# Kernel tuning notes

Hardware: AMD Instinct MI355X
Metric: run time of the kernel (lower is better)

## Reference

```python
import jax, jax.numpy as jnp
import numpy as np

VOL = (8, 56, 56)      # D, H, W
KER = (4, 7, 7)        # window size
SHIFT = (2, 3, 3)      # kernel // 2
C = 128                # embedding_dim
P = 256                # projection_dim
NH = 8                 # heads
HD = P // NH           # head dim = 32
HID = 3 * C            # mlp_ratio * C
B = 2
L = KER[0] * KER[1] * KER[2]                      # 196 tokens per window
NW = (VOL[0] // KER[0]) * (VOL[1] // KER[1]) * (VOL[2] // KER[2])  # 128 windows
EPS = 1e-5


def _rel_index():
    kd, kh, kw = KER
    coords = np.stack(np.meshgrid(np.arange(kd), np.arange(kh), np.arange(kw), indexing='ij'), 0).reshape(3, -1)
    rel = coords[:, :, None] - coords[:, None, :]
    rel = rel + np.array([kd - 1, kh - 1, kw - 1])[:, None, None]
    idx = rel[0] * (2 * kh - 1) * (2 * kw - 1) + rel[1] * (2 * kw - 1) + rel[2]
    return idx.astype(np.int32)  # [L, L]


def _shift_mask():
    D, H, W = VOL
    kd, kh, kw = KER
    sd, sh, sw = SHIFT
    img = np.zeros((D, H, W))
    cnt = 0
    for ds in (slice(0, -kd), slice(-kd, -sd), slice(-sd, None)):
        for hs in (slice(0, -kh), slice(-kh, -sh), slice(-sh, None)):
            for ws in (slice(0, -kw), slice(-kw, -sw), slice(-sw, None)):
                img[ds, hs, ws] = cnt
                cnt += 1
    win = img.reshape(D // kd, kd, H // kh, kh, W // kw, kw).transpose(0, 2, 4, 1, 3, 5).reshape(NW, L)
    diff = win[:, None, :] - win[:, :, None]
    return np.where(diff != 0, -100.0, 0.0).astype(np.float32)  # [NW, L, L]


def _partition(x):
    b = x.shape[0]
    kd, kh, kw = KER
    D, H, W = VOL
    x = x.reshape(b, D // kd, kd, H // kh, kh, W // kw, kw, C)
    x = x.transpose(0, 1, 3, 5, 2, 4, 6, 7)
    return x.reshape(b * NW, L, C)


def _reverse(x):
    b = x.shape[0] // NW
    kd, kh, kw = KER
    D, H, W = VOL
    x = x.reshape(b, D // kd, H // kh, W // kw, kd, kh, kw, C)
    x = x.transpose(0, 1, 4, 2, 5, 3, 6, 7)
    return x.reshape(b, D, H, W, C)


def _ln(x, g, b):
    mu = jnp.mean(x, -1, keepdims=True)
    var = jnp.mean(jnp.square(x - mu), -1, keepdims=True)
    return (x - mu) * jax.lax.rsqrt(var + EPS) * g + b


def setup_inputs() -> dict:
    key = jax.random.key(0)
    ks = jax.random.split(key, 16)
    s = 0.02
    d = {
        'query': jax.random.normal(ks[0], (B,) + VOL + (C,), jnp.float32),
        'key':   jax.random.normal(ks[1], (B,) + VOL + (C,), jnp.float32),
        'value': jax.random.normal(ks[2], (B,) + VOL + (C,), jnp.float32),
        'Wq': jax.random.normal(ks[3], (C, P), jnp.float32) * s,
        'bq': jnp.zeros((P,), jnp.float32),
        'Wk': jax.random.normal(ks[4], (C, P), jnp.float32) * s,
        'bk': jnp.zeros((P,), jnp.float32),
        'Wv': jax.random.normal(ks[5], (C, P), jnp.float32) * s,
        'bv': jnp.zeros((P,), jnp.float32),
        'Wo': jax.random.normal(ks[6], (P, C), jnp.float32) * s,
        'bo': jnp.zeros((C,), jnp.float32),
        'rel_table': jax.random.normal(ks[7], ((2 * KER[0] - 1) * (2 * KER[1] - 1) * (2 * KER[2] - 1), NH), jnp.float32) * s,
        'ln1_g': jnp.ones((C,), jnp.float32), 'ln1_b': jnp.zeros((C,), jnp.float32),
        'W1': jax.random.normal(ks[8], (C, HID), jnp.float32) * s,
        'b1': jnp.zeros((HID,), jnp.float32),
        'W2': jax.random.normal(ks[9], (HID, C), jnp.float32) * s,
        'b2': jnp.zeros((C,), jnp.float32),
        'ln2_g': jnp.ones((C,), jnp.float32), 'ln2_b': jnp.zeros((C,), jnp.float32),
        'rel_idx': jnp.asarray(_rel_index()),
        'attn_mask': jnp.asarray(_shift_mask()),
    }
    return d


def reference(query, key, value, Wq, bq, Wk, bk, Wv, bv, Wo, bo, rel_table,
              ln1_g, ln1_b, W1, b1, W2, b2, ln2_g, ln2_b, rel_idx, attn_mask):
    sd, sh, sw = SHIFT
    ax = (1, 2, 3)
    q = _partition(jnp.roll(query, (-sd, -sh, -sw), ax))
    k = _partition(jnp.roll(key,   (-sd, -sh, -sw), ax))
    v = _partition(jnp.roll(value, (-sd, -sh, -sw), ax))
    residual = q
    Bn = q.shape[0]
    qh = (q @ Wq + bq).reshape(Bn, L, NH, HD).transpose(0, 2, 1, 3)
    kh = (k @ Wk + bk).reshape(Bn, L, NH, HD).transpose(0, 2, 1, 3)
    vh = (v @ Wv + bv).reshape(Bn, L, NH, HD).transpose(0, 2, 1, 3)
    logits = jnp.einsum('bhqd,bhkd->bhqk', qh, kh) * (HD ** -0.5)
    bias = rel_table[rel_idx]                       # [L, L, NH]
    logits = logits + bias.transpose(2, 0, 1)[None]
    logits = logits.reshape(Bn // NW, NW, NH, L, L) + attn_mask[None, :, None]
    probs = jax.nn.softmax(logits.reshape(Bn, NH, L, L), axis=-1)
    ctx = jnp.einsum('bhqk,bhkd->bhqd', probs, vh).transpose(0, 2, 1, 3).reshape(Bn, L, P)
    attn = ctx @ Wo + bo
    attn = _ln(attn, ln1_g, ln1_b) + residual
    h = jax.nn.gelu(attn @ W1 + b1, approximate=False) @ W2 + b2
    out = _ln(h, ln2_g, ln2_b) + attn
    out = _reverse(out)
    return jnp.roll(out, (sd, sh, sw), ax)
```

## Files before the change

### kernel.cpp

```cpp
#include <hip/hip_runtime.h>
#include <math.h>

#define CC   128
#define PP   256
#define NHH  8
#define HDD  32
#define HIDD 384
#define LL   196
#define NWW  128
#define BNN  256
#define TT   50176
#define DV   8
#define HV   56
#define WV   56
#define KPAD 224
#define QPAD 224

typedef __attribute__((ext_vector_type(8))) short short8;
typedef __attribute__((ext_vector_type(4))) float f32x4;

#define WT_OQ 0
#define WT_OK 32768
#define WT_OV 65536
#define WT_OO 98304
#define WT_O1 131072
#define WT_O2 180224
#define WT_TOTAL 229376

__device__ __forceinline__ unsigned short f2bf(float x){
    unsigned u = __float_as_uint(x);
    u += 0x7FFFu + ((u >> 16) & 1u);
    return (unsigned short)(u >> 16);
}
__device__ __forceinline__ float bf2f(unsigned short h){
    return __uint_as_float(((unsigned)h) << 16);
}
__device__ __forceinline__ int pack2(unsigned short a, unsigned short b){
    return (int)(unsigned)a | ((int)(unsigned)b << 16);
}

__global__ __launch_bounds__(256) void k_wprep(
    const float* __restrict__ Wq, const float* __restrict__ Wk, const float* __restrict__ Wv,
    const float* __restrict__ Wo, const float* __restrict__ W1, const float* __restrict__ W2,
    short* __restrict__ WT)
{
    int t = blockIdx.x * 256 + threadIdx.x;
    if (t >= WT_TOTAL) return;
    float v;
    if (t < WT_OO) {
        int mat = t >> 15;
        int r = t & 32767;
        int n = r >> 7, kk = r & 127;
        const float* s = (mat == 0) ? Wq : (mat == 1) ? Wk : Wv;
        v = s[kk * PP + n];
    } else if (t < WT_O1) {
        int r = t - WT_OO;
        int n = r >> 8, kk = r & 255;
        v = Wo[kk * CC + n];
    } else if (t < WT_O2) {
        int r = t - WT_O1;
        int n = r >> 7, kk = r & 127;
        v = W1[kk * HIDD + n];
    } else {
        int r = t - WT_O2;
        int n = r / 384, kk = r - n * 384;
        v = W2[kk * CC + n];
    }
    unsigned short h = f2bf(v);
    float lo = v - bf2f(h);
    WT[t] = (short)h;
    WT[WT_TOTAL + t] = (short)f2bf(lo);
}

__global__ __launch_bounds__(256) void k_tab(const float* __restrict__ tbl,
                                             const int* __restrict__ idx,
                                             short* __restrict__ biasM)
{
    int t = blockIdx.x * 256 + threadIdx.x;
    if (t >= NHH * QPAD * KPAD) return;
    int k = t % KPAD, q = (t / KPAD) % QPAD, h = t / (KPAD * QPAD);
    float v = (q < LL && k < LL) ? tbl[idx[q * LL + k] * NHH + h] : -1.0e4f;
    biasM[t] = (short)f2bf(v);
}

__global__ __launch_bounds__(256) void k_maskpad(const float* __restrict__ msk,
                                                 short* __restrict__ maskM)
{
    int t = blockIdx.x * 256 + threadIdx.x;
    if (t >= NWW * QPAD * KPAD) return;
    int k = t % KPAD, q = (t / KPAD) % QPAD, w = t / (KPAD * QPAD);
    float v = (q < LL && k < LL) ? msk[(size_t)w * LL * LL + q * LL + k] : 0.f;
    maskM[t] = (short)f2bf(v);
}

template<int KD, int ND, int GELU, int QKV, int ASRC_BF16, int AOUT_BF16>
__global__ __launch_bounds__(256) void k_mgemm(
    const void* __restrict__ X0, const void* __restrict__ X1, const void* __restrict__ X2,
    const short* __restrict__ WhB, const short* __restrict__ WlB,
    const float* __restrict__ bb0, const float* __restrict__ bb1, const float* __restrict__ bb2,
    void* __restrict__ Y0, void* __restrict__ Y1, void* __restrict__ Y2,
    float* __restrict__ resid)
{
    __shared__ __align__(16) short Ah[128][40];
    __shared__ __align__(16) short Al[128][40];
    __shared__ __align__(16) short Bh[128][40];
    __shared__ __align__(16) short Bl[128][40];
    __shared__ int s_off[128];

    const int tid = threadIdx.x;
    const int m0 = blockIdx.x * 128;
    const int c0 = blockIdx.y * 128;
    const int z = QKV ? blockIdx.z : 0;
    const void* __restrict__ X  = (z == 0) ? X0 : (z == 1) ? X1 : X2;
    const float* __restrict__ bb = (z == 0) ? bb0 : (z == 1) ? bb1 : bb2;
    void* __restrict__ Y         = (z == 0) ? Y0 : (z == 1) ? Y1 : Y2;
    const short* __restrict__ Wh = WhB + (QKV ? z * 32768 : 0);
    const short* __restrict__ Wl = WlB + (QKV ? z * 32768 : 0);

    if (QKV && tid < 128) {
        int m = m0 + tid;
        int l = m % LL, bw = m / LL;
        int w = bw & (NWW - 1), b = bw >> 7;
        int wd = w >> 6, wh = (w >> 3) & 7, ww = w & 7;
        int td = l / 49, r = l % 49, th = r / 7, tw = r % 7;
        int d  = wd * 4 + td + 2;  if (d  >= DV) d  -= DV;
        int hh = wh * 7 + th + 3;  if (hh >= HV) hh -= HV;
        int wc2 = ww * 7 + tw + 3; if (wc2 >= WV) wc2 -= WV;
        s_off[tid] = (((b * DV + d) * HV + hh) * WV + wc2) * CC;
    }

    const int wid = tid >> 6, lane = tid & 63;
    const int wr = wid >> 1, wc = wid & 1;
    const int lrow = lane & 15, kg = lane >> 4;

    f32x4 acc[4][4];
    f32x4 zero = {0.f, 0.f, 0.f, 0.f};
#pragma unroll
    for (int m = 0; m < 4; m++)
#pragma unroll
        for (int n = 0; n < 4; n++) acc[m][n] = zero;

    const int arow = tid >> 1, ahalf = tid & 1;

    for (int kc = 0; kc < KD / 32; kc++) {
        __syncthreads();
        if constexpr (ASRC_BF16) {
            const short* gp = (const short*)X + (size_t)(m0 + arow) * KD + kc * 32 + ahalf * 16;
            *(int4*)&Ah[arow][ahalf * 16]     = *(const int4*)(gp);
            *(int4*)&Ah[arow][ahalf * 16 + 8] = *(const int4*)(gp + 8);
        } else {
            const float* gp;
            if (QKV) gp = (const float*)X + s_off[arow] + kc * 32 + ahalf * 16;
            else     gp = (const float*)X + (size_t)(m0 + arow) * KD + kc * 32 + ahalf * 16;
            float4 a0 = *(const float4*)(gp);
            float4 a1 = *(const float4*)(gp + 4);
            float4 a2 = *(const float4*)(gp + 8);
            float4 a3 = *(const float4*)(gp + 12);
            if (QKV && z == 0 && blockIdx.y == 0) {
                float* rp = resid + (size_t)(m0 + arow) * CC + kc * 32 + ahalf * 16;
                *(float4*)(rp) = a0; *(float4*)(rp + 4) = a1;
                *(float4*)(rp + 8) = a2; *(float4*)(rp + 12) = a3;
            }
            float f[16] = {a0.x,a0.y,a0.z,a0.w, a1.x,a1.y,a1.z,a1.w,
                           a2.x,a2.y,a2.z,a2.w, a3.x,a3.y,a3.z,a3.w};
            int hi[8], lo[8];
#pragma unroll
            for (int e = 0; e < 8; e++) {
                unsigned short h0 = f2bf(f[2*e]),   h1 = f2bf(f[2*e+1]);
                float l0 = f[2*e] - bf2f(h0), l1 = f[2*e+1] - bf2f(h1);
                hi[e] = pack2(h0, h1);
                lo[e] = pack2(f2bf(l0), f2bf(l1));
            }
            int4* dh = (int4*)&Ah[arow][ahalf * 16];
            dh[0] = make_int4(hi[0], hi[1], hi[2], hi[3]);
            dh[1] = make_int4(hi[4], hi[5], hi[6], hi[7]);
            int4* dl = (int4*)&Al[arow][ahalf * 16];
            dl[0] = make_int4(lo[0], lo[1], lo[2], lo[3]);
            dl[1] = make_int4(lo[4], lo[5], lo[6], lo[7]);
        }
        {
            const short* sh = Wh + (size_t)(c0 + arow) * KD + kc * 32 + ahalf * 16;
            const short* sl = Wl + (size_t)(c0 + arow) * KD + kc * 32 + ahalf * 16;
            int4* dh = (int4*)&Bh[arow][ahalf * 16];
            dh[0] = *(const int4*)(sh); dh[1] = *(const int4*)(sh + 8);
            int4* dl = (int4*)&Bl[arow][ahalf * 16];
            dl[0] = *(const int4*)(sl); dl[1] = *(const int4*)(sl + 8);
        }
        __syncthreads();

        short8 afh[4], afl[4], bfh[4], bfl[4];
#pragma unroll
        for (int m = 0; m < 4; m++) {
            int r = wr * 64 + m * 16 + lrow;
            afh[m] = *(const short8*)&Ah[r][kg * 8];
            if constexpr (!ASRC_BF16) afl[m] = *(const short8*)&Al[r][kg * 8];
        }
#pragma unroll
        for (int n = 0; n < 4; n++) {
            int cidx = wc * 64 + n * 16 + lrow;
            bfh[n] = *(const short8*)&Bh[cidx][kg * 8];
            bfl[n] = *(const short8*)&Bl[cidx][kg * 8];
        }
#pragma unroll
        for (int m = 0; m < 4; m++)
#pragma unroll
            for (int n = 0; n < 4; n++) {
                acc[m][n] = __builtin_amdgcn_mfma_f32_16x16x32_bf16(afh[m], bfh[n], acc[m][n], 0, 0, 0);
                acc[m][n] = __builtin_amdgcn_mfma_f32_16x16x32_bf16(afh[m], bfl[n], acc[m][n], 0, 0, 0);
                if constexpr (!ASRC_BF16)
                    acc[m][n] = __builtin_amdgcn_mfma_f32_16x16x32_bf16(afl[m], bfh[n], acc[m][n], 0, 0, 0);
            }
    }

#pragma unroll
    for (int n = 0; n < 4; n++) {
        int col = c0 + wc * 64 + n * 16 + lrow;
        float bv = bb[col];
#pragma unroll
        for (int m = 0; m < 4; m++) {
#pragma unroll
            for (int rg = 0; rg < 4; rg++) {
                int r = wr * 64 + m * 16 + kg * 4 + rg;
                float x = acc[m][n][rg] + bv;
                if (GELU) x = 0.5f * x * (1.f + erff(x * 0.70710678118654752f));
                int tok = m0 + r;
                if constexpr (QKV) {
                    int bw = (unsigned)tok / LL;
                    int l  = tok - bw * LL;
                    int head = col >> 5, hd = col & 31;
                    short* Yb = (short*)Y;
                    if (z == 2)
                        Yb[(((size_t)bw * NHH + head) * HDD + hd) * KPAD + l] = (short)f2bf(x);
                    else
                        Yb[(((size_t)bw * NHH + head) * LL + l) * HDD + hd] = (short)f2bf(x);
                } else if constexpr (AOUT_BF16) {
                    ((short*)Y)[(size_t)tok * ND + col] = (short)f2bf(x);
                } else {
                    ((float*)Y)[(size_t)tok * ND + col] = x;
                }
            }
        }
    }
}

__global__ __launch_bounds__(448) void k_attn2(
    const short* __restrict__ Qb, const short* __restrict__ Kb, const short* __restrict__ Vt,
    const short* __restrict__ biasM, const short* __restrict__ maskM,
    float* __restrict__ ctx)
{
    __shared__ __align__(16) short Kf[14 * 64 * 8];
    __shared__ __align__(16) short Vf[14 * 64 * 8];
    __shared__ __align__(16) short Pf[7 * 7 * 64 * 8];
    const int h = blockIdx.x, bn = blockIdx.y;
    const int w = bn & (NWW - 1);
    const int tid = threadIdx.x;
    const size_t kvb = (size_t)bn * NHH + h;

    for (int f = tid; f < 14 * 64; f += 448) {
        int ln = f & 63, kt = f >> 6;
        int ktok = kt * 16 + (ln & 15);
        int hd0 = (ln >> 4) * 8;
        short8 val = {0,0,0,0,0,0,0,0};
        if (ktok < LL) val = *(const short8*)(Kb + (kvb * LL + ktok) * HDD + hd0);
        *(short8*)(Kf + f * 8) = val;
    }
    for (int f = tid; f < 14 * 64; f += 448) {
        int ln = f & 63, t2 = f >> 6;
        int dt = t2 & 1, kt32 = t2 >> 1;
        int d = dt * 16 + (ln & 15);
        int k0 = kt32 * 32 + (ln >> 4) * 8;
        *(short8*)(Vf + f * 8) = *(const short8*)(Vt + (kvb * HDD + d) * KPAD + k0);
    }
    __syncthreads();

    const int wv = tid >> 6, lane = tid & 63;
    const int qcol = lane & 15, kg = lane >> 4;
    const int qb = wv * 32;
    short* const myP = Pf + wv * 3584;
    const float scale = 0.17677669529663687f;

    for (int qt = 0; qt < 2; qt++) {
        const int q = qb + qt * 16 + qcol;
        const int qr = (q < LL) ? q : (LL - 1);
        short8 qf = *(const short8*)(Qb + (kvb * LL + qr) * HDD + kg * 8);

        f32x4 st[14];
#pragma unroll
        for (int kt = 0; kt < 14; kt++) {
            short8 kf = *(const short8*)(Kf + (kt * 64 + lane) * 8);
            f32x4 zz = {0.f, 0.f, 0.f, 0.f};
            st[kt] = __builtin_amdgcn_mfma_f32_16x16x32_bf16(kf, qf, zz, 0, 0, 0);
        }

        float psum = 0.f;
        const short* bp = biasM + ((size_t)h * QPAD + q) * KPAD;
        const short* mp = maskM + ((size_t)w * QPAD + q) * KPAD;
#pragma unroll
        for (int kt = 0; kt < 14; kt++) {
            int k0 = kt * 16 + kg * 4;
            short4 b4 = *(const short4*)(bp + k0);
            short4 m4 = *(const short4*)(mp + k0);
            float p0 = __expf(st[kt][0] * scale + bf2f((unsigned short)b4.x) + bf2f((unsigned short)m4.x));
            float p1 = __expf(st[kt][1] * scale + bf2f((unsigned short)b4.y) + bf2f((unsigned short)m4.y));
            float p2 = __expf(st[kt][2] * scale + bf2f((unsigned short)b4.z) + bf2f((unsigned short)m4.z));
            float p3 = __expf(st[kt][3] * scale + bf2f((unsigned short)b4.w) + bf2f((unsigned short)m4.w));
            st[kt][0] = p0; st[kt][1] = p1; st[kt][2] = p2; st[kt][3] = p3;
            psum += (p0 + p1) + (p2 + p3);
        }
        psum += __shfl_xor(psum, 16);
        psum += __shfl_xor(psum, 32);
        const float inv = 1.f / psum;

#pragma unroll
        for (int kt = 0; kt < 14; kt++) {
            int I0 = pack2(f2bf(st[kt][0] * inv), f2bf(st[kt][1] * inv));
            int I1 = pack2(f2bf(st[kt][2] * inv), f2bf(st[kt][3] * inv));
            int kg_r = (kt & 1) * 2 + (kg >> 1);
            int slot = (kt >> 1) * 64 + kg_r * 16 + qcol;
            *(int2*)(myP + slot * 8 + (kg & 1) * 4) = make_int2(I0, I1);
        }

        f32x4 o0 = {0.f, 0.f, 0.f, 0.f}, o1 = {0.f, 0.f, 0.f, 0.f};
#pragma unroll
        for (int kt32 = 0; kt32 < 7; kt32++) {
            short8 pf = *(const short8*)(myP + (kt32 * 64 + lane) * 8);
            short8 v0 = *(const short8*)(Vf + ((kt32 * 2 + 0) * 64 + lane) * 8);
            short8 v1 = *(const short8*)(Vf + ((kt32 * 2 + 1) * 64 + lane) * 8);
            o0 = __builtin_amdgcn_mfma_f32_16x16x32_bf16(v0, pf, o0, 0, 0, 0);
            o1 = __builtin_amdgcn_mfma_f32_16x16x32_bf16(v1, pf, o1, 0, 0, 0);
        }
        if (q < LL) {
            float* cp = ctx + ((size_t)bn * LL + q) * PP + h * HDD;
#pragma unroll
            for (int rg = 0; rg < 4; rg++) {
                cp[kg * 4 + rg]      = o0[rg];
                cp[16 + kg * 4 + rg] = o1[rg];
            }
        }
    }
}

__global__ __launch_bounds__(256) void k_ln_add(
    const float* __restrict__ X, const float* __restrict__ gg, const float* __restrict__ bb,
    const float* __restrict__ res, float* __restrict__ Y)
{
    const int row = blockIdx.x * 4 + (threadIdx.x >> 6);
    const int lane = threadIdx.x & 63;
    const float2 v = ((const float2*)(X + (size_t)row * CC))[lane];
    float s = v.x + v.y, s2 = v.x * v.x + v.y * v.y;
#pragma unroll
    for (int m = 1; m < 64; m <<= 1) { s += __shfl_xor(s, m); s2 += __shfl_xor(s2, m); }
    const float mean = s * 0.0078125f;
    const float var  = s2 * 0.0078125f - mean * mean;
    const float rinv = rsqrtf(var + 1e-5f);
    const float2 g2 = ((const float2*)gg)[lane];
    const float2 b2 = ((const float2*)bb)[lane];
    const float2 r2 = ((const float2*)(res + (size_t)row * CC))[lane];
    float2 o;
    o.x = (v.x - mean) * rinv * g2.x + b2.x + r2.x;
    o.y = (v.y - mean) * rinv * g2.y + b2.y + r2.y;
    ((float2*)(Y + (size_t)row * CC))[lane] = o;
}

__global__ __launch_bounds__(256) void k_ln2_scatter(
    const float* __restrict__ X, const float* __restrict__ gg, const float* __restrict__ bb,
    const float* __restrict__ res, float* __restrict__ out)
{
    const int row = blockIdx.x * 4 + (threadIdx.x >> 6);
    const int lane = threadIdx.x & 63;
    const float2 v = ((const float2*)(X + (size_t)row * CC))[lane];
    float s = v.x + v.y, s2 = v.x * v.x + v.y * v.y;
#pragma unroll
    for (int m = 1; m < 64; m <<= 1) { s += __shfl_xor(s, m); s2 += __shfl_xor(s2, m); }
    const float mean = s * 0.0078125f;
    const float var  = s2 * 0.0078125f - mean * mean;
    const float rinv = rsqrtf(var + 1e-5f);
    const float2 g2 = ((const float2*)gg)[lane];
    const float2 b2 = ((const float2*)bb)[lane];
    const float2 r2 = ((const float2*)(res + (size_t)row * CC))[lane];
    float2 o;
    o.x = (v.x - mean) * rinv * g2.x + b2.x + r2.x;
    o.y = (v.y - mean) * rinv * g2.y + b2.y + r2.y;

    int l = row % LL, bw = row / LL;
    int w = bw & (NWW - 1), b = bw >> 7;
    int wd = w >> 6, wh = (w >> 3) & 7, ww = w & 7;
    int td = l / 49, r = l % 49, th = r / 7, tw = r % 7;
    int d  = wd * 4 + td + 2;  if (d  >= DV) d  -= DV;
    int hh = wh * 7 + th + 3;  if (hh >= HV) hh -= HV;
    int wc = ww * 7 + tw + 3;  if (wc >= WV) wc -= WV;
    size_t dest = (((size_t)(b * DV + d) * HV + hh) * WV + wc) * CC;
    ((float2*)(out + dest))[lane] = o;
}

extern "C" void kernel_launch(void* const* d_in, const int* in_sizes, int n_in,
                              void* d_out, int out_size, void* d_ws, size_t ws_size,
                              hipStream_t stream)
{
    (void)in_sizes; (void)n_in; (void)out_size;
    const float* q    = (const float*)d_in[0];
    const float* k    = (const float*)d_in[1];
    const float* v    = (const float*)d_in[2];
    const float* bq   = (const float*)d_in[4];
    const float* bk   = (const float*)d_in[6];
    const float* bv   = (const float*)d_in[8];
    const float* bo   = (const float*)d_in[10];
    const float* rtab = (const float*)d_in[11];
    const float* g1   = (const float*)d_in[12];
    const float* b1n  = (const float*)d_in[13];
    const float* b1m  = (const float*)d_in[15];
    const float* b2m  = (const float*)d_in[17];
    const float* g2   = (const float*)d_in[18];
    const float* b2n  = (const float*)d_in[19];
    const int*   ridx = (const int*)d_in[20];
    const float* msk  = (const float*)d_in[21];
    float* out = (float*)d_out;
    char*  base = (char*)d_ws;

    float* resid = (float*)(base);
    short* Qb    = (short*)(base + 25690112);
    short* Kb2   = (short*)(base + 51380224);
    short* Vt    = (short*)(base + 77070336);
    float* ctxb  = (float*)(base + 106430464);
    short* biasM = (short*)(base + 157810688);
    short* maskM = (short*)(base + 158613504);
    float* h2    = (float*)(base + 171458560);
    float* proj1 = (float*)(base + 25690112);
    float* attnb = (float*)(base + 51380224);
    short* h1    = (short*)(base + 77070336);

    short* WT = (short*)d_out;

    const size_t need = 197148672;
    if (ws_size < need) return;

    k_wprep<<<dim3(WT_TOTAL / 256), dim3(256), 0, stream>>>(
        (const float*)d_in[3], (const float*)d_in[5], (const float*)d_in[7],
        (const float*)d_in[9], (const float*)d_in[14], (const float*)d_in[16], WT);
    k_tab<<<dim3(NHH * QPAD * KPAD / 256), dim3(256), 0, stream>>>(rtab, ridx, biasM);
    k_maskpad<<<dim3(NWW * QPAD * KPAD / 256), dim3(256), 0, stream>>>(msk, maskM);

    k_mgemm<128, 256, 0, 1, 0, 0><<<dim3(TT / 128, 2, 3), dim3(256), 0, stream>>>(
        q, k, v, WT + WT_OQ, WT + WT_TOTAL + WT_OQ,
        bq, bk, bv, Qb, Kb2, Vt, resid);

    k_attn2<<<dim3(NHH, BNN), dim3(448), 0, stream>>>(Qb, Kb2, Vt, biasM, maskM, ctxb);

    k_mgemm<256, 128, 0, 0, 0, 0><<<dim3(TT / 128, 1), dim3(256), 0, stream>>>(
        ctxb, ctxb, ctxb, WT + WT_OO, WT + WT_TOTAL + WT_OO,
        bo, bo, bo, proj1, proj1, proj1, nullptr);

    k_ln_add<<<dim3(TT / 4), dim3(256), 0, stream>>>(proj1, g1, b1n, resid, attnb);

    k_mgemm<128, 384, 1, 0, 0, 1><<<dim3(TT / 128, 3), dim3(256), 0, stream>>>(
        attnb, attnb, attnb, WT + WT_O1, WT + WT_TOTAL + WT_O1,
        b1m, b1m, b1m, h1, h1, h1, nullptr);

    k_mgemm<384, 128, 0, 0, 1, 0><<<dim3(TT / 128, 1), dim3(256), 0, stream>>>(
        h1, h1, h1, WT + WT_O2, WT + WT_TOTAL + WT_O2,
        b2m, b2m, b2m, h2, h2, h2, nullptr);

    k_ln2_scatter<<<dim3(TT / 4), dim3(256), 0, stream>>>(h2, g2, b2n, attnb, out);
}
```

Before: 450.5 us.

## Pre-pack operands into MFMA fragment panels and rebuild GEMMs with direct-to-LDS loads

A separate gather kernel now rolls, partitions and splits Q/K/V inputs into hi/lo bf16 planes stored in MFMA fragment order. Weights, the attention context, the LN1 output and the MLP hidden activation are written in the same panel layout. The new GEMM uses 512-thread blocks with larger tiles and global_load_lds to copy whole fragment chunks straight into shared memory, with no in-kernel conversion or padding. The bias and mask tables get a parity-shifted key layout to match the new attention input format. The cost is an extra gather pass, a larger workspace and more panel-format writes in the epilogues.

```diff
diff --git a/kernel.cpp b/kernel.cpp
--- a/kernel.cpp
+++ b/kernel.cpp
@@ -15,18 +15,34 @@
 #define WV   56
 #define KPAD 224
 #define QPAD 224
+#define TB16 3136
 
 typedef __attribute__((ext_vector_type(8))) short short8;
 typedef __attribute__((ext_vector_type(4))) float f32x4;
 
 #define WT_OQ 0
-#define WT_OK 32768
-#define WT_OV 65536
 #define WT_OO 98304
 #define WT_O1 131072
 #define WT_O2 180224
 #define WT_TOTAL 229376
 
+#define O_RESID  0u
+#define O_GP     25690112u
+#define O_QF     102760448u
+#define O_KF     132120576u
+#define O_VF     161480704u
+#define O_BIAS   190840832u
+#define O_MASK   192446464u
+#define O_CTXP   25690112u
+#define O_PROJ1  51380224u
+#define O_ATTNB  102760448u
+#define O_ATTP   132120576u
+#define O_H1P    161480704u
+#define O_H2     77070336u
+#define GP_PL    6422528
+#define ATT_PL   6422528
+#define WS_NEED  205291520u
+
 __device__ __forceinline__ unsigned short f2bf(float x){
     unsigned u = __float_as_uint(x);
     u += 0x7FFFu + ((u >> 16) & 1u);
@@ -38,238 +54,304 @@
 __device__ __forceinline__ int pack2(unsigned short a, unsigned short b){
     return (int)(unsigned)a | ((int)(unsigned)b << 16);
 }
-
-__global__ __launch_bounds__(256) void k_wprep(
+__device__ __forceinline__ void gload16(const void* g, void* l){
+    __builtin_amdgcn_global_load_lds(
+        (const __attribute__((address_space(1))) void*)g,
+        (__attribute__((address_space(3))) void*)l, 16, 0, 0);
+}
+__device__ __forceinline__ int roll_off(int tok){
+    int l = tok % LL, bw = tok / LL;
+    int w = bw & (NWW - 1), b = bw >> 7;
+    int wd = w >> 6, wh = (w >> 3) & 7, ww = w & 7;
+    int td = l / 49, r = l % 49, th = r / 7, tw = r % 7;
+    int d  = wd * 4 + td + 2;  if (d  >= DV) d  -= DV;
+    int hh = wh * 7 + th + 3;  if (hh >= HV) hh -= HV;
+    int wc = ww * 7 + tw + 3;  if (wc >= WV) wc -= WV;
+    return (((b * DV + d) * HV + hh) * WV + wc) * CC;
+}
+
+__global__ __launch_bounds__(256) void k_wprep2(
     const float* __restrict__ Wq, const float* __restrict__ Wk, const float* __restrict__ Wv,
     const float* __restrict__ Wo, const float* __restrict__ W1, const float* __restrict__ W2,
     short* __restrict__ WT)
 {
     int t = blockIdx.x * 256 + threadIdx.x;
     if (t >= WT_TOTAL) return;
-    float v;
-    if (t < WT_OO) {
-        int mat = t >> 15;
-        int r = t & 32767;
-        int n = r >> 7, kk = r & 127;
-        const float* s = (mat == 0) ? Wq : (mat == 1) ? Wk : Wv;
-        v = s[kk * PP + n];
-    } else if (t < WT_O1) {
-        int r = t - WT_OO;
-        int n = r >> 8, kk = r & 255;
-        v = Wo[kk * CC + n];
-    } else if (t < WT_O2) {
-        int r = t - WT_O1;
-        int n = r >> 7, kk = r & 127;
-        v = W1[kk * HIDD + n];
-    } else {
-        int r = t - WT_O2;
-        int n = r / 384, kk = r - n * 384;
-        v = W2[kk * CC + n];
-    }
+    const float* src; int ndf, rel;
+    if (t < WT_OO)      { src = (t >> 15) == 0 ? Wq : ((t >> 15) == 1 ? Wk : Wv); ndf = 256; rel = t & 32767; }
+    else if (t < WT_O1) { src = Wo; ndf = 128; rel = t - WT_OO; }
+    else if (t < WT_O2) { src = W1; ndf = 384; rel = t - WT_O1; }
+    else                { src = W2; ndf = 128; rel = t - WT_O2; }
+    int per_kc = (ndf / 16) * 512;
+    int kc = rel / per_kc, r2 = rel % per_kc;
+    int nblk = r2 >> 9, ln = (r2 >> 3) & 63, e = r2 & 7;
+    int n = nblk * 16 + (ln & 15);
+    int k = kc * 32 + (ln >> 4) * 8 + e;
+    float v = src[(size_t)k * ndf + n];
     unsigned short h = f2bf(v);
-    float lo = v - bf2f(h);
     WT[t] = (short)h;
-    WT[WT_TOTAL + t] = (short)f2bf(lo);
-}
-
-__global__ __launch_bounds__(256) void k_tab(const float* __restrict__ tbl,
-                                             const int* __restrict__ idx,
-                                             short* __restrict__ biasM)
+    WT[WT_TOTAL + t] = (short)f2bf(v - bf2f(h));
+}
+
+__global__ __launch_bounds__(256) void k_gather(
+    const float* __restrict__ qs, const float* __restrict__ ks, const float* __restrict__ vs,
+    short* __restrict__ Gp, float* __restrict__ resid)
+{
+    const int tid = threadIdx.x;
+    const int tok = blockIdx.x * 16 + (tid >> 4);
+    const int j = tid & 15;
+    const int off = roll_off(tok) + j * 8;
+    const int kc = j >> 2, k8 = j & 3;
+    const size_t slot = (((size_t)kc * TB16 + (tok >> 4)) * 64 + (tok & 15) + k8 * 16) * 8;
+    const float* srcs[3] = {qs, ks, vs};
+#pragma unroll
+    for (int z = 0; z < 3; z++) {
+        float4 a0 = *(const float4*)(srcs[z] + off);
+        float4 a1 = *(const float4*)(srcs[z] + off + 4);
+        float f[8] = {a0.x,a0.y,a0.z,a0.w,a1.x,a1.y,a1.z,a1.w};
+        short8 hi, lo;
+#pragma unroll
+        for (int e = 0; e < 8; e++) {
+            unsigned short h = f2bf(f[e]);
+            hi[e] = (short)h;
+            lo[e] = (short)f2bf(f[e] - bf2f(h));
+        }
+        *(short8*)(Gp + (size_t)(z * 2 + 0) * GP_PL + slot) = hi;
+        *(short8*)(Gp + (size_t)(z * 2 + 1) * GP_PL + slot) = lo;
+        if (z == 0) {
+            float* rp = resid + (size_t)tok * CC + j * 8;
+            *(float4*)rp = a0; *(float4*)(rp + 4) = a1;
+        }
+    }
+}
+
+__global__ __launch_bounds__(256) void k_tab2(const float* __restrict__ tbl,
+                                              const int* __restrict__ idx,
+                                              short* __restrict__ biasM)
 {
     int t = blockIdx.x * 256 + threadIdx.x;
-    if (t >= NHH * QPAD * KPAD) return;
-    int k = t % KPAD, q = (t / KPAD) % QPAD, h = t / (KPAD * QPAD);
-    float v = (q < LL && k < LL) ? tbl[idx[q * LL + k] * NHH + h] : -1.0e4f;
+    if (t >= NHH * 2 * QPAD * KPAD) return;
+    int ks = t % KPAD, q = (t / KPAD) % QPAD;
+    int par = (t / (KPAD * QPAD)) & 1, h = t / (KPAD * QPAD * 2);
+    int l = ks - 4 * par;
+    float v = (q < LL && l >= 0 && l < LL) ? tbl[idx[q * LL + l] * NHH + h] : -1.0e4f;
     biasM[t] = (short)f2bf(v);
 }
 
-__global__ __launch_bounds__(256) void k_maskpad(const float* __restrict__ msk,
-                                                 short* __restrict__ maskM)
+__global__ __launch_bounds__(256) void k_maskpad2(const float* __restrict__ msk,
+                                                  short* __restrict__ maskM)
 {
     int t = blockIdx.x * 256 + threadIdx.x;
     if (t >= NWW * QPAD * KPAD) return;
-    int k = t % KPAD, q = (t / KPAD) % QPAD, w = t / (KPAD * QPAD);
-    float v = (q < LL && k < LL) ? msk[(size_t)w * LL * LL + q * LL + k] : 0.f;
+    int ks = t % KPAD, q = (t / KPAD) % QPAD, w = t / (KPAD * QPAD);
+    int l = ks - 4 * (w & 1);
+    float v = (q < LL && l >= 0 && l < LL) ? msk[((size_t)w * LL + q) * LL + l] : 0.f;
     maskM[t] = (short)f2bf(v);
 }
 
-template<int KD, int ND, int GELU, int QKV, int ASRC_BF16, int AOUT_BF16>
-__global__ __launch_bounds__(256) void k_mgemm(
-    const void* __restrict__ X0, const void* __restrict__ X1, const void* __restrict__ X2,
+template<int MT, int NT, int KD, int APL, int NDF, int EPI>
+__global__ __launch_bounds__(512) void mgemm2(
+    const short* __restrict__ A0, const short* __restrict__ A1,
     const short* __restrict__ WhB, const short* __restrict__ WlB,
-    const float* __restrict__ bb0, const float* __restrict__ bb1, const float* __restrict__ bb2,
-    void* __restrict__ Y0, void* __restrict__ Y1, void* __restrict__ Y2,
-    float* __restrict__ resid)
-{
-    __shared__ __align__(16) short Ah[128][40];
-    __shared__ __align__(16) short Al[128][40];
-    __shared__ __align__(16) short Bh[128][40];
-    __shared__ __align__(16) short Bl[128][40];
-    __shared__ int s_off[128];
+    const float* __restrict__ b0, const float* __restrict__ b1, const float* __restrict__ b2,
+    void* __restrict__ Y0, void* __restrict__ Y1, void* __restrict__ Y2)
+{
+    constexpr int ACH = APL * MT / 16;
+    constexpr int NCH = ACH + 2 * (NT / 16);
+    __shared__ __align__(16) short smem[NCH * 512];
 
     const int tid = threadIdx.x;
-    const int m0 = blockIdx.x * 128;
-    const int c0 = blockIdx.y * 128;
-    const int z = QKV ? blockIdx.z : 0;
-    const void* __restrict__ X  = (z == 0) ? X0 : (z == 1) ? X1 : X2;
-    const float* __restrict__ bb = (z == 0) ? bb0 : (z == 1) ? bb1 : bb2;
-    void* __restrict__ Y         = (z == 0) ? Y0 : (z == 1) ? Y1 : Y2;
-    const short* __restrict__ Wh = WhB + (QKV ? z * 32768 : 0);
-    const short* __restrict__ Wl = WlB + (QKV ? z * 32768 : 0);
-
-    if (QKV && tid < 128) {
-        int m = m0 + tid;
-        int l = m % LL, bw = m / LL;
-        int w = bw & (NWW - 1), b = bw >> 7;
-        int wd = w >> 6, wh = (w >> 3) & 7, ww = w & 7;
-        int td = l / 49, r = l % 49, th = r / 7, tw = r % 7;
-        int d  = wd * 4 + td + 2;  if (d  >= DV) d  -= DV;
-        int hh = wh * 7 + th + 3;  if (hh >= HV) hh -= HV;
-        int wc2 = ww * 7 + tw + 3; if (wc2 >= WV) wc2 -= WV;
-        s_off[tid] = (((b * DV + d) * HV + hh) * WV + wc2) * CC;
-    }
-
     const int wid = tid >> 6, lane = tid & 63;
-    const int wr = wid >> 1, wc = wid & 1;
+    constexpr int WN = NT / 64;
+    const int wm = wid / WN, wn = wid % WN;
     const int lrow = lane & 15, kg = lane >> 4;
+    const int m0 = blockIdx.x * MT;
+    const int c0 = blockIdx.y * NT;
+    const int z = (EPI == 1) ? blockIdx.z : 0;
+
+    const short* Ap0 = (EPI == 1) ? A0 + (size_t)(z * 2) * GP_PL : A0;
+    const short* Ap1 = (EPI == 1) ? A0 + (size_t)(z * 2 + 1) * GP_PL : A1;
+    const short* Wh = WhB + (EPI == 1 ? z * 32768 : 0);
+    const short* Wl = WlB + (EPI == 1 ? z * 32768 : 0);
+    const float* bb = (z == 0) ? b0 : (z == 1) ? b1 : b2;
 
     f32x4 acc[4][4];
-    f32x4 zero = {0.f, 0.f, 0.f, 0.f};
-#pragma unroll
-    for (int m = 0; m < 4; m++)
-#pragma unroll
-        for (int n = 0; n < 4; n++) acc[m][n] = zero;
-
-    const int arow = tid >> 1, ahalf = tid & 1;
+    f32x4 zero = {0.f,0.f,0.f,0.f};
+#pragma unroll
+    for (int i = 0; i < 4; i++)
+#pragma unroll
+        for (int j = 0; j < 4; j++) acc[i][j] = zero;
 
     for (int kc = 0; kc < KD / 32; kc++) {
         __syncthreads();
-        if constexpr (ASRC_BF16) {
-            const short* gp = (const short*)X + (size_t)(m0 + arow) * KD + kc * 32 + ahalf * 16;
-            *(int4*)&Ah[arow][ahalf * 16]     = *(const int4*)(gp);
-            *(int4*)&Ah[arow][ahalf * 16 + 8] = *(const int4*)(gp + 8);
-        } else {
-            const float* gp;
-            if (QKV) gp = (const float*)X + s_off[arow] + kc * 32 + ahalf * 16;
-            else     gp = (const float*)X + (size_t)(m0 + arow) * KD + kc * 32 + ahalf * 16;
-            float4 a0 = *(const float4*)(gp);
-            float4 a1 = *(const float4*)(gp + 4);
-            float4 a2 = *(const float4*)(gp + 8);
-            float4 a3 = *(const float4*)(gp + 12);
-            if (QKV && z == 0 && blockIdx.y == 0) {
-                float* rp = resid + (size_t)(m0 + arow) * CC + kc * 32 + ahalf * 16;
-                *(float4*)(rp) = a0; *(float4*)(rp + 4) = a1;
-                *(float4*)(rp + 8) = a2; *(float4*)(rp + 12) = a3;
-            }
-            float f[16] = {a0.x,a0.y,a0.z,a0.w, a1.x,a1.y,a1.z,a1.w,
-                           a2.x,a2.y,a2.z,a2.w, a3.x,a3.y,a3.z,a3.w};
-            int hi[8], lo[8];
-#pragma unroll
-            for (int e = 0; e < 8; e++) {
-                unsigned short h0 = f2bf(f[2*e]),   h1 = f2bf(f[2*e+1]);
-                float l0 = f[2*e] - bf2f(h0), l1 = f[2*e+1] - bf2f(h1);
-                hi[e] = pack2(h0, h1);
-                lo[e] = pack2(f2bf(l0), f2bf(l1));
-            }
-            int4* dh = (int4*)&Ah[arow][ahalf * 16];
-            dh[0] = make_int4(hi[0], hi[1], hi[2], hi[3]);
-            dh[1] = make_int4(hi[4], hi[5], hi[6], hi[7]);
-            int4* dl = (int4*)&Al[arow][ahalf * 16];
-            dl[0] = make_int4(lo[0], lo[1], lo[2], lo[3]);
-            dl[1] = make_int4(lo[4], lo[5], lo[6], lo[7]);
-        }
-        {
-            const short* sh = Wh + (size_t)(c0 + arow) * KD + kc * 32 + ahalf * 16;
-            const short* sl = Wl + (size_t)(c0 + arow) * KD + kc * 32 + ahalf * 16;
-            int4* dh = (int4*)&Bh[arow][ahalf * 16];
-            dh[0] = *(const int4*)(sh); dh[1] = *(const int4*)(sh + 8);
-            int4* dl = (int4*)&Bl[arow][ahalf * 16];
-            dl[0] = *(const int4*)(sl); dl[1] = *(const int4*)(sl + 8);
+        for (int c = wid; c < NCH; c += 8) {
+            const short* src;
+            if (c < ACH) {
+                int pl = c / (MT / 16), fb = c % (MT / 16);
+                src = (pl ? Ap1 : Ap0) + ((size_t)kc * TB16 + m0 / 16 + fb) * 512;
+            } else {
+                int c2 = c - ACH;
+                int pl = c2 / (NT / 16), fb = c2 % (NT / 16);
+                src = (pl ? Wl : Wh) + ((size_t)kc * (NDF / 16) + c0 / 16 + fb) * 512;
+            }
+            gload16(src + lane * 8, &smem[c * 512]);
         }
         __syncthreads();
 
-        short8 afh[4], afl[4], bfh[4], bfl[4];
-#pragma unroll
-        for (int m = 0; m < 4; m++) {
-            int r = wr * 64 + m * 16 + lrow;
-            afh[m] = *(const short8*)&Ah[r][kg * 8];
-            if constexpr (!ASRC_BF16) afl[m] = *(const short8*)&Al[r][kg * 8];
-        }
-#pragma unroll
-        for (int n = 0; n < 4; n++) {
-            int cidx = wc * 64 + n * 16 + lrow;
-            bfh[n] = *(const short8*)&Bh[cidx][kg * 8];
-            bfl[n] = *(const short8*)&Bl[cidx][kg * 8];
-        }
-#pragma unroll
-        for (int m = 0; m < 4; m++)
-#pragma unroll
-            for (int n = 0; n < 4; n++) {
-                acc[m][n] = __builtin_amdgcn_mfma_f32_16x16x32_bf16(afh[m], bfh[n], acc[m][n], 0, 0, 0);
-                acc[m][n] = __builtin_amdgcn_mfma_f32_16x16x32_bf16(afh[m], bfl[n], acc[m][n], 0, 0, 0);
-                if constexpr (!ASRC_BF16)
-                    acc[m][n] = __builtin_amdgcn_mfma_f32_16x16x32_bf16(afl[m], bfh[n], acc[m][n], 0, 0, 0);
-            }
-    }
-
-#pragma unroll
-    for (int n = 0; n < 4; n++) {
-        int col = c0 + wc * 64 + n * 16 + lrow;
-        float bv = bb[col];
-#pragma unroll
-        for (int m = 0; m < 4; m++) {
-#pragma unroll
-            for (int rg = 0; rg < 4; rg++) {
-                int r = wr * 64 + m * 16 + kg * 4 + rg;
-                float x = acc[m][n][rg] + bv;
-                if (GELU) x = 0.5f * x * (1.f + erff(x * 0.70710678118654752f));
-                int tok = m0 + r;
-                if constexpr (QKV) {
-                    int bw = (unsigned)tok / LL;
-                    int l  = tok - bw * LL;
-                    int head = col >> 5, hd = col & 31;
-                    short* Yb = (short*)Y;
-                    if (z == 2)
-                        Yb[(((size_t)bw * NHH + head) * HDD + hd) * KPAD + l] = (short)f2bf(x);
-                    else
-                        Yb[(((size_t)bw * NHH + head) * LL + l) * HDD + hd] = (short)f2bf(x);
-                } else if constexpr (AOUT_BF16) {
-                    ((short*)Y)[(size_t)tok * ND + col] = (short)f2bf(x);
+        short8 bh[4], bl[4];
+#pragma unroll
+        for (int j = 0; j < 4; j++) {
+            bh[j] = *(const short8*)&smem[(ACH + wn * 4 + j) * 512 + lane * 8];
+            bl[j] = *(const short8*)&smem[(ACH + NT / 16 + wn * 4 + j) * 512 + lane * 8];
+        }
+#pragma unroll
+        for (int i = 0; i < 4; i++) {
+            short8 ah = *(const short8*)&smem[(wm * 4 + i) * 512 + lane * 8];
+            short8 al;
+            if constexpr (APL == 2) al = *(const short8*)&smem[(MT / 16 + wm * 4 + i) * 512 + lane * 8];
+#pragma unroll
+            for (int j = 0; j < 4; j++) {
+                acc[i][j] = __builtin_amdgcn_mfma_f32_16x16x32_bf16(ah, bh[j], acc[i][j], 0, 0, 0);
+                acc[i][j] = __builtin_amdgcn_mfma_f32_16x16x32_bf16(ah, bl[j], acc[i][j], 0, 0, 0);
+                if constexpr (APL == 2)
+                    acc[i][j] = __builtin_amdgcn_mfma_f32_16x16x32_bf16(al, bh[j], acc[i][j], 0, 0, 0);
+            }
+        }
+    }
+    __syncthreads();
+
+    float bv[4];
+#pragma unroll
+    for (int j = 0; j < 4; j++) bv[j] = bb[c0 + wn * 64 + j * 16 + lrow];
+
+    if constexpr (EPI == 0) {
+        float* Y = (float*)Y0;
+#pragma unroll
+        for (int j = 0; j < 4; j++) {
+            int col = c0 + wn * 64 + j * 16 + lrow;
+#pragma unroll
+            for (int i = 0; i < 4; i++)
+#pragma unroll
+                for (int rg = 0; rg < 4; rg++) {
+                    int tok = m0 + wm * 64 + i * 16 + kg * 4 + rg;
+                    Y[(size_t)tok * NDF + col] = acc[i][j][rg] + bv[j];
+                }
+        }
+        return;
+    }
+
+    short* bw = smem + wid * 2048;
+
+    if constexpr (EPI == 1) if (z == 2) {
+        short* VF = (short*)Y2;
+#pragma unroll
+        for (int hp = 0; hp < 2; hp++) {
+#pragma unroll
+            for (int jj = 0; jj < 2; jj++) {
+                int j = hp * 2 + jj;
+                int colL = jj * 16 + lrow;
+#pragma unroll
+                for (int i = 0; i < 4; i++) {
+                    int tokL0 = i * 16 + kg * 4;
+                    short4 pk;
+                    pk.x = (short)f2bf(acc[i][j][0] + bv[j]);
+                    pk.y = (short)f2bf(acc[i][j][1] + bv[j]);
+                    pk.z = (short)f2bf(acc[i][j][2] + bv[j]);
+                    pk.w = (short)f2bf(acc[i][j][3] + bv[j]);
+                    *(short4*)&bw[colL * 64 + (tokL0 ^ ((colL & 7) << 3))] = pk;
+                }
+            }
+            int head = (wn * 64 + hp * 32) >> 5;
+#pragma unroll
+            for (int it = 0; it < 4; it++) {
+                int d = lrow + (it & 1) * 16;
+                int ti0 = (kg + (it >> 1) * 4) * 8;
+                short8 v = *(const short8*)&bw[d * 64 + (ti0 ^ ((d & 7) << 3))];
+                int tok0 = m0 + wm * 64 + ti0;
+                int bnA = tok0 / LL, bnB = (tok0 + 7) / LL;
+                if (bnA == bnB) {
+                    int ks0 = tok0 - bnA * LL + 4 * (bnA & 1);
+                    size_t o = ((((size_t)bnA * NHH + head) * 14 + (ks0 >> 5) * 2 + (d >> 4)) * 64
+                                + (d & 15) + ((ks0 >> 3) & 3) * 16) * 8;
+                    *(short8*)(VF + o) = v;
                 } else {
-                    ((float*)Y)[(size_t)tok * ND + col] = x;
+#pragma unroll
+                    for (int e = 0; e < 8; e++) {
+                        int tok = tok0 + e;
+                        int bn = tok / LL;
+                        int ks = tok - bn * LL + 4 * (bn & 1);
+                        size_t o = ((((size_t)bn * NHH + head) * 14 + (ks >> 5) * 2 + (d >> 4)) * 64
+                                    + (d & 15) + ((ks >> 3) & 3) * 16) * 8 + (ks & 7);
+                        VF[o] = v[e];
+                    }
                 }
             }
+            __builtin_amdgcn_sched_barrier(0);
+        }
+        return;
+    }
+
+    if constexpr (EPI == 1 || EPI == 2) {
+        short* F = (EPI == 2) ? (short*)Y0 : (short*)(z == 0 ? Y0 : Y1);
+#pragma unroll
+        for (int hp = 0; hp < 2; hp++) {
+#pragma unroll
+            for (int jj = 0; jj < 2; jj++) {
+                int j = hp * 2 + jj;
+#pragma unroll
+                for (int i = 0; i < 4; i++)
+#pragma unroll
+                    for (int rg = 0; rg < 4; rg++) {
+                        int tokL = i * 16 + kg * 4 + rg;
+                        int colL = jj * 16 + lrow;
+                        float x = acc[i][j][rg] + bv[j];
+                        if constexpr (EPI == 2)
+                            x = 0.5f * x * (1.f + erff(x * 0.70710678118654752f));
+                        bw[tokL * 32 + (colL ^ (kg << 3))] = (short)f2bf(x);
+                    }
+            }
+#pragma unroll
+            for (int it = 0; it < 4; it++) {
+                int tokL = it * 16 + lrow;
+                int swr = (tokL >> 2) & 3;
+                short8 v = *(const short8*)&bw[tokL * 32 + ((kg * 8) ^ (swr << 3))];
+                int tok = m0 + wm * 64 + tokL;
+                if constexpr (EPI == 1) {
+                    int head = (wn * 64 + hp * 32) >> 5;
+                    int bn = tok / LL, l = tok - bn * LL;
+                    int slot = (z == 1) ? l + 4 * (bn & 1) : l;
+                    size_t o = ((((size_t)bn * NHH + head) * 14 + (slot >> 4)) * 64
+                                + (slot & 15) + kg * 16) * 8;
+                    *(short8*)(F + o) = v;
+                } else {
+                    int kglob = c0 + wn * 64 + hp * 32 + kg * 8;
+                    size_t o = (((size_t)(kglob >> 5) * TB16 + (tok >> 4)) * 64
+                                + (tok & 15) + ((kglob & 31) >> 3) * 16) * 8;
+                    *(short8*)(F + o) = v;
+                }
+            }
+            __builtin_amdgcn_sched_barrier(0);
         }
     }
 }
 
 __global__ __launch_bounds__(448) void k_attn2(
-    const short* __restrict__ Qb, const short* __restrict__ Kb, const short* __restrict__ Vt,
+    const short* __restrict__ QF, const short* __restrict__ KF, const short* __restrict__ VF,
     const short* __restrict__ biasM, const short* __restrict__ maskM,
-    float* __restrict__ ctx)
+    short* __restrict__ CTXp)
 {
     __shared__ __align__(16) short Kf[14 * 64 * 8];
     __shared__ __align__(16) short Vf[14 * 64 * 8];
     __shared__ __align__(16) short Pf[7 * 7 * 64 * 8];
     const int h = blockIdx.x, bn = blockIdx.y;
     const int w = bn & (NWW - 1);
+    const int par = bn & 1;
     const int tid = threadIdx.x;
     const size_t kvb = (size_t)bn * NHH + h;
 
     for (int f = tid; f < 14 * 64; f += 448) {
-        int ln = f & 63, kt = f >> 6;
-        int ktok = kt * 16 + (ln & 15);
-        int hd0 = (ln >> 4) * 8;
-        short8 val = {0,0,0,0,0,0,0,0};
-        if (ktok < LL) val = *(const short8*)(Kb + (kvb * LL + ktok) * HDD + hd0);
-        *(short8*)(Kf + f * 8) = val;
-    }
-    for (int f = tid; f < 14 * 64; f += 448) {
-        int ln = f & 63, t2 = f >> 6;
-        int dt = t2 & 1, kt32 = t2 >> 1;
-        int d = dt * 16 + (ln & 15);
-        int k0 = kt32 * 32 + (ln >> 4) * 8;
-        *(short8*)(Vf + f * 8) = *(const short8*)(Vt + (kvb * HDD + d) * KPAD + k0);
+        *(short8*)(Kf + f * 8) = *(const short8*)(KF + (kvb * 14 * 64 + f) * 8);
+        *(short8*)(Vf + f * 8) = *(const short8*)(VF + (kvb * 14 * 64 + f) * 8);
     }
     __syncthreads();
 
@@ -281,19 +363,18 @@
 
     for (int qt = 0; qt < 2; qt++) {
         const int q = qb + qt * 16 + qcol;
-        const int qr = (q < LL) ? q : (LL - 1);
-        short8 qf = *(const short8*)(Qb + (kvb * LL + qr) * HDD + kg * 8);
+        short8 qf = *(const short8*)(QF + ((kvb * 14 + (q >> 4)) * 64 + (q & 15) + kg * 16) * 8);
 
         f32x4 st[14];
 #pragma unroll
         for (int kt = 0; kt < 14; kt++) {
             short8 kf = *(const short8*)(Kf + (kt * 64 + lane) * 8);
-            f32x4 zz = {0.f, 0.f, 0.f, 0.f};
+            f32x4 zz = {0.f,0.f,0.f,0.f};
             st[kt] = __builtin_amdgcn_mfma_f32_16x16x32_bf16(kf, qf, zz, 0, 0, 0);
         }
 
         float psum = 0.f;
-        const short* bp = biasM + ((size_t)h * QPAD + q) * KPAD;
+        const short* bp = biasM + (((size_t)h * 2 + par) * QPAD + q) * KPAD;
         const short* mp = maskM + ((size_t)w * QPAD + q) * KPAD;
 #pragma unroll
         for (int kt = 0; kt < 14; kt++) {
@@ -320,7 +401,7 @@
             *(int2*)(myP + slot * 8 + (kg & 1) * 4) = make_int2(I0, I1);
         }
 
-        f32x4 o0 = {0.f, 0.f, 0.f, 0.f}, o1 = {0.f, 0.f, 0.f, 0.f};
+        f32x4 o0 = {0.f,0.f,0.f,0.f}, o1 = {0.f,0.f,0.f,0.f};
 #pragma unroll
         for (int kt32 = 0; kt32 < 7; kt32++) {
             short8 pf = *(const short8*)(myP + (kt32 * 64 + lane) * 8);
@@ -329,20 +410,84 @@
             o0 = __builtin_amdgcn_mfma_f32_16x16x32_bf16(v0, pf, o0, 0, 0, 0);
             o1 = __builtin_amdgcn_mfma_f32_16x16x32_bf16(v1, pf, o1, 0, 0, 0);
         }
-        if (q < LL) {
-            float* cp = ctx + ((size_t)bn * LL + q) * PP + h * HDD;
-#pragma unroll
-            for (int rg = 0; rg < 4; rg++) {
-                cp[kg * 4 + rg]      = o0[rg];
-                cp[16 + kg * 4 + rg] = o1[rg];
-            }
-        }
-    }
-}
-
-__global__ __launch_bounds__(256) void k_ln_add(
+        __builtin_amdgcn_sched_barrier(0);
+
+        {
+            int sw = (qcol & 7) << 2;
+            short4 s0, s1;
+            s0.x = (short)f2bf(o0[0]); s0.y = (short)f2bf(o0[1]);
+            s0.z = (short)f2bf(o0[2]); s0.w = (short)f2bf(o0[3]);
+            s1.x = (short)f2bf(o1[0]); s1.y = (short)f2bf(o1[1]);
+            s1.z = (short)f2bf(o1[2]); s1.w = (short)f2bf(o1[3]);
+            *(short4*)&myP[qcol * 32 + ((kg * 4) ^ sw)] = s0;
+            *(short4*)&myP[qcol * 32 + ((16 + kg * 4) ^ sw)] = s1;
+        }
+        {
+            int qr = qb + qt * 16 + (lane & 15);
+            int k8 = lane >> 4;
+            int sw = ((lane & 15) & 7) << 2;
+            short4 a = *(const short4*)&myP[(lane & 15) * 32 + ((k8 * 8) ^ sw)];
+            short4 b = *(const short4*)&myP[(lane & 15) * 32 + ((k8 * 8 + 4) ^ sw)];
+            if (qr < LL) {
+                int tok = bn * LL + qr;
+                short8 o = {a.x, a.y, a.z, a.w, b.x, b.y, b.z, b.w};
+                size_t dst = (((size_t)h * TB16 + (tok >> 4)) * 64 + (tok & 15) + k8 * 16) * 8;
+                *(short8*)(CTXp + dst) = o;
+            }
+        }
+        __builtin_amdgcn_sched_barrier(0);
+    }
+}
+
+__global__ __launch_bounds__(256) void k_ln_panel(
+    const float* __restrict__ X, const float* __restrict__ gg, const float* __restrict__ bbv,
+    const float* __restrict__ res, float* __restrict__ Y, short* __restrict__ ATTp)
+{
+    const int row = blockIdx.x * 16 + (threadIdx.x >> 4);
+    const int j = threadIdx.x & 15;
+    const float4 x0 = *(const float4*)(X + (size_t)row * CC + j * 8);
+    const float4 x1 = *(const float4*)(X + (size_t)row * CC + j * 8 + 4);
+    float s  = x0.x+x0.y+x0.z+x0.w + x1.x+x1.y+x1.z+x1.w;
+    float s2 = x0.x*x0.x+x0.y*x0.y+x0.z*x0.z+x0.w*x0.w
+             + x1.x*x1.x+x1.y*x1.y+x1.z*x1.z+x1.w*x1.w;
+#pragma unroll
+    for (int m = 1; m < 16; m <<= 1) { s += __shfl_xor(s, m); s2 += __shfl_xor(s2, m); }
+    const float mean = s * 0.0078125f;
+    const float var  = s2 * 0.0078125f - mean * mean;
+    const float rinv = rsqrtf(var + 1e-5f);
+    const float4 g0 = *(const float4*)(gg + j * 8);
+    const float4 g1 = *(const float4*)(gg + j * 8 + 4);
+    const float4 b0 = *(const float4*)(bbv + j * 8);
+    const float4 b1 = *(const float4*)(bbv + j * 8 + 4);
+    const float4 r0 = *(const float4*)(res + (size_t)row * CC + j * 8);
+    const float4 r1 = *(const float4*)(res + (size_t)row * CC + j * 8 + 4);
+    float o[8];
+    o[0] = (x0.x-mean)*rinv*g0.x + b0.x + r0.x;
+    o[1] = (x0.y-mean)*rinv*g0.y + b0.y + r0.y;
+    o[2] = (x0.z-mean)*rinv*g0.z + b0.z + r0.z;
+    o[3] = (x0.w-mean)*rinv*g0.w + b0.w + r0.w;
+    o[4] = (x1.x-mean)*rinv*g1.x + b1.x + r1.x;
+    o[5] = (x1.y-mean)*rinv*g1.y + b1.y + r1.y;
+    o[6] = (x1.z-mean)*rinv*g1.z + b1.z + r1.z;
+    o[7] = (x1.w-mean)*rinv*g1.w + b1.w + r1.w;
+    float* yp = Y + (size_t)row * CC + j * 8;
+    *(float4*)yp = make_float4(o[0],o[1],o[2],o[3]);
+    *(float4*)(yp+4) = make_float4(o[4],o[5],o[6],o[7]);
+    short8 hi, lo;
+#pragma unroll
+    for (int e = 0; e < 8; e++) {
+        unsigned short hh = f2bf(o[e]);
+        hi[e] = (short)hh;
+        lo[e] = (short)f2bf(o[e] - bf2f(hh));
+    }
+    size_t slot = (((size_t)(j >> 2) * TB16 + (row >> 4)) * 64 + (row & 15) + (j & 3) * 16) * 8;
+    *(short8*)(ATTp + slot) = hi;
+    *(short8*)(ATTp + ATT_PL + slot) = lo;
+}
+
+__global__ __launch_bounds__(256) void k_ln2_scatter(
     const float* __restrict__ X, const float* __restrict__ gg, const float* __restrict__ bb,
-    const float* __restrict__ res, float* __restrict__ Y)
+    const float* __restrict__ res, float* __restrict__ out)
 {
     const int row = blockIdx.x * 4 + (threadIdx.x >> 6);
     const int lane = threadIdx.x & 63;
@@ -359,38 +504,7 @@
     float2 o;
     o.x = (v.x - mean) * rinv * g2.x + b2.x + r2.x;
     o.y = (v.y - mean) * rinv * g2.y + b2.y + r2.y;
-    ((float2*)(Y + (size_t)row * CC))[lane] = o;
-}
-
-__global__ __launch_bounds__(256) void k_ln2_scatter(
-    const float* __restrict__ X, const float* __restrict__ gg, const float* __restrict__ bb,
-    const float* __restrict__ res, float* __restrict__ out)
-{
-    const int row = blockIdx.x * 4 + (threadIdx.x >> 6);
-    const int lane = threadIdx.x & 63;
-    const float2 v = ((const float2*)(X + (size_t)row * CC))[lane];
-    float s = v.x + v.y, s2 = v.x * v.x + v.y * v.y;
-#pragma unroll
-    for (int m = 1; m < 64; m <<= 1) { s += __shfl_xor(s, m); s2 += __shfl_xor(s2, m); }
-    const float mean = s * 0.0078125f;
-    const float var  = s2 * 0.0078125f - mean * mean;
-    const float rinv = rsqrtf(var + 1e-5f);
-    const float2 g2 = ((const float2*)gg)[lane];
-    const float2 b2 = ((const float2*)bb)[lane];
-    const float2 r2 = ((const float2*)(res + (size_t)row * CC))[lane];
-    float2 o;
-    o.x = (v.x - mean) * rinv * g2.x + b2.x + r2.x;
-    o.y = (v.y - mean) * rinv * g2.y + b2.y + r2.y;
-
-    int l = row % LL, bw = row / LL;
-    int w = bw & (NWW - 1), b = bw >> 7;
-    int wd = w >> 6, wh = (w >> 3) & 7, ww = w & 7;
-    int td = l / 49, r = l % 49, th = r / 7, tw = r % 7;
-    int d  = wd * 4 + td + 2;  if (d  >= DV) d  -= DV;
-    int hh = wh * 7 + th + 3;  if (hh >= HV) hh -= HV;
-    int wc = ww * 7 + tw + 3;  if (wc >= WV) wc -= WV;
-    size_t dest = (((size_t)(b * DV + d) * HV + hh) * WV + wc) * CC;
-    ((float2*)(out + dest))[lane] = o;
+    ((float2*)(out + roll_off(row)))[lane] = o;
 }
 
 extern "C" void kernel_launch(void* const* d_in, const int* in_sizes, int n_in,
@@ -417,48 +531,49 @@
     float* out = (float*)d_out;
     char*  base = (char*)d_ws;
 
-    float* resid = (float*)(base);
-    short* Qb    = (short*)(base + 25690112);
-    short* Kb2   = (short*)(base + 51380224);
-    short* Vt    = (short*)(base + 77070336);
-    float* ctxb  = (float*)(base + 106430464);
-    short* biasM = (short*)(base + 157810688);
-    short* maskM = (short*)(base + 158613504);
-    float* h2    = (float*)(base + 171458560);
-    float* proj1 = (float*)(base + 25690112);
-    float* attnb = (float*)(base + 51380224);
-    short* h1    = (short*)(base + 77070336);
-
+    float* resid = (float*)(base + O_RESID);
+    short* Gp    = (short*)(base + O_GP);
+    short* QF    = (short*)(base + O_QF);
+    short* KF    = (short*)(base + O_KF);
+    short* VF    = (short*)(base + O_VF);
+    short* biasM = (short*)(base + O_BIAS);
+    short* maskM = (short*)(base + O_MASK);
+    short* CTXp  = (short*)(base + O_CTXP);
+    float* proj1 = (float*)(base + O_PROJ1);
+    float* attnb = (float*)(base + O_ATTNB);
+    short* ATTp  = (short*)(base + O_ATTP);
+    short* H1p   = (short*)(base + O_H1P);
+    float* h2    = (float*)(base + O_H2);
     short* WT = (short*)d_out;
 
-    const size_t need = 197148672;
-    if (ws_size < need) return;
-
-    k_wprep<<<dim3(WT_TOTAL / 256), dim3(256), 0, stream>>>(
+    if (ws_size < (size_t)WS_NEED) return;
+
+    k_wprep2<<<dim3(WT_TOTAL / 256), dim3(256), 0, stream>>>(
         (const float*)d_in[3], (const float*)d_in[5], (const float*)d_in[7],
         (const float*)d_in[9], (const float*)d_in[14], (const float*)d_in[16], WT);
-    k_tab<<<dim3(NHH * QPAD * KPAD / 256), dim3(256), 0, stream>>>(rtab, ridx, biasM);
-    k_maskpad<<<dim3(NWW * QPAD * KPAD / 256), dim3(256), 0, stream>>>(msk, maskM);
-
-    k_mgemm<128, 256, 0, 1, 0, 0><<<dim3(TT / 128, 2, 3), dim3(256), 0, stream>>>(
-        q, k, v, WT + WT_OQ, WT + WT_TOTAL + WT_OQ,
-        bq, bk, bv, Qb, Kb2, Vt, resid);
-
-    k_attn2<<<dim3(NHH, BNN), dim3(448), 0, stream>>>(Qb, Kb2, Vt, biasM, maskM, ctxb);
-
-    k_mgemm<256, 128, 0, 0, 0, 0><<<dim3(TT / 128, 1), dim3(256), 0, stream>>>(
-        ctxb, ctxb, ctxb, WT + WT_OO, WT + WT_TOTAL + WT_OO,
-        bo, bo, bo, proj1, proj1, proj1, nullptr);
-
-    k_ln_add<<<dim3(TT / 4), dim3(256), 0, stream>>>(proj1, g1, b1n, resid, attnb);
-
-    k_mgemm<128, 384, 1, 0, 0, 1><<<dim3(TT / 128, 3), dim3(256), 0, stream>>>(
-        attnb, attnb, attnb, WT + WT_O1, WT + WT_TOTAL + WT_O1,
-        b1m, b1m, b1m, h1, h1, h1, nullptr);
-
-    k_mgemm<384, 128, 0, 0, 1, 0><<<dim3(TT / 128, 1), dim3(256), 0, stream>>>(
-        h1, h1, h1, WT + WT_O2, WT + WT_TOTAL + WT_O2,
-        b2m, b2m, b2m, h2, h2, h2, nullptr);
+    k_gather<<<dim3(TB16), dim3(256), 0, stream>>>(q, k, v, Gp, resid);
+    k_tab2<<<dim3(NHH * 2 * QPAD * KPAD / 256), dim3(256), 0, stream>>>(rtab, ridx, biasM);
+    k_maskpad2<<<dim3(NWW * QPAD * KPAD / 256), dim3(256), 0, stream>>>(msk, maskM);
+
+    mgemm2<128, 256, 128, 2, 256, 1><<<dim3(TT / 128, 1, 3), dim3(512), 0, stream>>>(
+        Gp, nullptr, WT + WT_OQ, WT + WT_TOTAL + WT_OQ,
+        bq, bk, bv, QF, KF, VF);
+
+    k_attn2<<<dim3(NHH, BNN), dim3(448), 0, stream>>>(QF, KF, VF, biasM, maskM, CTXp);
+
+    mgemm2<256, 128, 256, 1, 128, 0><<<dim3(TT / 256, 1, 1), dim3(512), 0, stream>>>(
+        CTXp, nullptr, WT + WT_OO, WT + WT_TOTAL + WT_OO,
+        bo, bo, bo, proj1, nullptr, nullptr);
+
+    k_ln_panel<<<dim3(TB16), dim3(256), 0, stream>>>(proj1, g1, b1n, resid, attnb, ATTp);
+
+    mgemm2<256, 128, 128, 2, 384, 2><<<dim3(TT / 256, 3, 1), dim3(512), 0, stream>>>(
+        ATTp, ATTp + ATT_PL, WT + WT_O1, WT + WT_TOTAL + WT_O1,
+        b1m, b1m, b1m, H1p, nullptr, nullptr);
+
+    mgemm2<256, 128, 384, 1, 128, 0><<<dim3(TT / 256, 1, 1), dim3(512), 0, stream>>>(
+        H1p, nullptr, WT + WT_O2, WT + WT_TOTAL + WT_O2,
+        b2m, b2m, b2m, h2, nullptr, nullptr);
 
     k_ln2_scatter<<<dim3(TT / 4), dim3(256), 0, stream>>>(h2, g2, b2n, attnb, out);
 }
```

Measured after the change: 442.4 us. No clear change (-1.8%).
